# Performance work log

Measured on AMD Instinct MI355X. Metric: run time of the kernel, lower is better.

The kernel has to match this reference:

```python
import jax, jax.numpy as jnp
import numpy as np

POOL_SIZE = 100
TOP_K = 5
EPS = 1e-12

def l2_normalize(x, axis):
    # matches module: x * rsqrt(max(sum(x^2), eps))
    sq = jnp.sum(x * x, axis=axis, keepdims=True)
    return x * jax.lax.rsqrt(jnp.maximum(sq, EPS))

def setup_inputs() -> dict:
    key = jax.random.key(0)
    k1, k2 = jax.random.split(key)
    x_embed = jax.random.normal(k1, (256, 512, 768), dtype=jnp.float32)
    # prompt_key init 'uniform' -> U(-1, 1)
    prompt_key = jax.random.uniform(k2, (POOL_SIZE, 768), dtype=jnp.float32, minval=-1.0, maxval=1.0)
    return {"x_embed": x_embed, "prompt_key": prompt_key}

def reference(x_embed, prompt_key):
    B = x_embed.shape[0]
    # embedding_key == 'cls' with cls_features=None -> max over sequence dim
    x_embed_mean = jnp.max(x_embed, axis=1)                      # [B, D]
    prompt_norm = l2_normalize(prompt_key, axis=1)               # [P, D]
    x_embed_norm = l2_normalize(x_embed_mean, axis=1)            # [B, D]
    similarity = jnp.matmul(x_embed_norm, prompt_norm.T)         # [B, P]
    _, idx = jax.lax.top_k(similarity, TOP_K)                    # [B, K] (batchwise_prompt=False)
    selected_key = prompt_norm[idx]                              # [B, K, D] gather
    sim = selected_key * x_embed_norm[:, None, :]                # [B, K, D]
    reduce_sim = jnp.sum(sim) / B
    return similarity, selected_key, reduce_sim, idx
```

## Files before the change

kernel.cpp:

```cpp
#include <hip/hip_runtime.h>
#include <float.h>

#define B 256
#define S 512
#define D 768
#define P 100
#define K 5
#define SPLIT 4
#define SCHUNK (S / SPLIT)
#define D4 (D / 4)

#define PART_OFF 0
#define PN_OFF   (SPLIT * B * D)
#define XN_OFF   (PN_OFF + P * D)

#define SIM_OFF 0
#define SEL_OFF (B * P)
#define RS_OFF  (SEL_OFF + B * K * D)
#define IDX_OFF (RS_OFF + 1)

__device__ inline float4 fmax4(float4 a, float4 b) {
    return make_float4(fmaxf(a.x, b.x), fmaxf(a.y, b.y),
                       fmaxf(a.z, b.z), fmaxf(a.w, b.w));
}

__global__ __launch_bounds__(192) void k_partmax(const float* __restrict__ x,
                                                 float* __restrict__ ws) {
    const int blk = blockIdx.x;
    const int b  = blk >> 2;
    const int sp = blk & 3;
    const int t  = threadIdx.x;
    const float4* src = (const float4*)(x + (size_t)b * S * D)
                        + (size_t)(sp * SCHUNK) * D4 + t;
    float4 m0 = make_float4(-FLT_MAX, -FLT_MAX, -FLT_MAX, -FLT_MAX);
    float4 m1 = m0, m2 = m0, m3 = m0;
    for (int s = 0; s < SCHUNK; s += 4) {
        float4 a0 = src[(size_t)(s + 0) * D4];
        float4 a1 = src[(size_t)(s + 1) * D4];
        float4 a2 = src[(size_t)(s + 2) * D4];
        float4 a3 = src[(size_t)(s + 3) * D4];
        m0 = fmax4(m0, a0);
        m1 = fmax4(m1, a1);
        m2 = fmax4(m2, a2);
        m3 = fmax4(m3, a3);
    }
    float4 m = fmax4(fmax4(m0, m1), fmax4(m2, m3));
    ((float4*)(ws + PART_OFF))[(size_t)(sp * B + b) * D4 + t] = m;
}

__device__ inline float block_sum_192(float v, float* lds) {
    for (int off = 32; off; off >>= 1) v += __shfl_down(v, off);
    const int lane = threadIdx.x & 63;
    const int w = threadIdx.x >> 6;
    if (lane == 0) lds[w] = v;
    __syncthreads();
    float tot = lds[0] + lds[1] + lds[2];
    __syncthreads();
    return tot;
}

__device__ inline float precise_rsqrt(float tot) {
    float x = fmaxf(tot, 1e-12f);
    float r = rsqrtf(x);
    r = r * (1.5f - 0.5f * x * r * r);
    return r;
}

__global__ __launch_bounds__(192) void k_prompt_norm(const float* __restrict__ pk,
                                                     float* __restrict__ ws) {
    __shared__ float lds[3];
    const int p = blockIdx.x, t = threadIdx.x;
    float4 v = ((const float4*)pk)[(size_t)p * D4 + t];
    float sq = v.x * v.x + v.y * v.y + v.z * v.z + v.w * v.w;
    float tot = block_sum_192(sq, lds);
    float r = precise_rsqrt(tot);
    ((float4*)(ws + PN_OFF))[(size_t)p * D4 + t] =
        make_float4(v.x * r, v.y * r, v.z * r, v.w * r);
}

__global__ __launch_bounds__(192) void k_xnorm(float* __restrict__ ws,
                                               float* __restrict__ out) {
    __shared__ float lds[3];
    const int b = blockIdx.x, t = threadIdx.x;
    const float4* part = (const float4*)(ws + PART_OFF);
    float4 m = part[(size_t)b * D4 + t];
    for (int sp = 1; sp < SPLIT; ++sp)
        m = fmax4(m, part[(size_t)(sp * B + b) * D4 + t]);
    float sq = m.x * m.x + m.y * m.y + m.z * m.z + m.w * m.w;
    float tot = block_sum_192(sq, lds);
    float r = precise_rsqrt(tot);
    ((float4*)(ws + XN_OFF))[(size_t)b * D4 + t] =
        make_float4(m.x * r, m.y * r, m.z * r, m.w * r);
    if (b == 0 && t == 0) out[RS_OFF] = 0.0f;
}

__global__ __launch_bounds__(256) void k_sim_topk(const float* __restrict__ ws,
                                                  float* __restrict__ out) {
    __shared__ float xs[D];
    __shared__ float simbuf[P];
    __shared__ float topv[K];
    __shared__ int   topi[K];
    const int b = blockIdx.x, t = threadIdx.x;
    const int w = t >> 6, lane = t & 63;

    const float* xn = ws + XN_OFF + (size_t)b * D;
    if (t < D4) ((float4*)xs)[t] = ((const float4*)xn)[t];
    __syncthreads();

    const float* pn = ws + PN_OFF;
    for (int j = 0; j < 25; ++j) {
        const int p = w + 4 * j;
        float acc = 0.f;
        #pragma unroll
        for (int jj = 0; jj < 12; ++jj) {
            const int d = lane + 64 * jj;
            acc += pn[(size_t)p * D + d] * xs[d];
        }
        for (int off = 32; off; off >>= 1) acc += __shfl_down(acc, off);
        if (lane == 0) {
            simbuf[p] = acc;
            out[SIM_OFF + (size_t)b * P + p] = acc;
        }
    }
    __syncthreads();

    if (w == 0) {
        float v0 = (lane < P) ? simbuf[lane] : -FLT_MAX;
        int   i0 = lane;
        int   i1 = lane + 64;
        float v1 = (i1 < P) ? simbuf[i1] : -FLT_MAX;
        for (int k = 0; k < K; ++k) {
            float bv; int bi;
            if (v0 > v1 || (v0 == v1 && i0 < i1)) { bv = v0; bi = i0; }
            else                                  { bv = v1; bi = i1; }
            for (int off = 32; off; off >>= 1) {
                float ov = __shfl_xor(bv, off);
                int   oi = __shfl_xor(bi, off);
                if (ov > bv || (ov == bv && oi < bi)) { bv = ov; bi = oi; }
            }
            if (lane == 0) { topv[k] = bv; topi[k] = bi; }
            if (bi == i0) v0 = -FLT_MAX;
            else if (bi == i1) v1 = -FLT_MAX;
        }
    }
    __syncthreads();

    if (t < K) out[IDX_OFF + (size_t)b * K + t] = (float)topi[t];

    if (t == 0) {
        float s = topv[0] + topv[1] + topv[2] + topv[3] + topv[4];
        atomicAdd(out + RS_OFF, s * (1.0f / (float)B));
    }

    const float4* pn4 = (const float4*)pn;
    float4* sel4 = (float4*)(out + SEL_OFF) + (size_t)b * (K * D4);
    for (int i = t; i < K * D4; i += 256) {
        const int k = i / D4;
        const int e = i - k * D4;
        sel4[i] = pn4[(size_t)topi[k] * D4 + e];
    }
}

extern "C" void kernel_launch(void* const* d_in, const int* in_sizes, int n_in,
                              void* d_out, int out_size, void* d_ws, size_t ws_size,
                              hipStream_t stream) {
    const float* x_embed    = (const float*)d_in[0];
    const float* prompt_key = (const float*)d_in[1];
    float* out = (float*)d_out;
    float* ws  = (float*)d_ws;

    k_partmax<<<B * SPLIT, 192, 0, stream>>>(x_embed, ws);
    k_prompt_norm<<<P, 192, 0, stream>>>(prompt_key, ws);
    k_xnorm<<<B, 192, 0, stream>>>(ws, out);
    k_sim_topk<<<B, 256, 0, stream>>>(ws, out);
}
```

Baseline: 611.4 us.

## Fuse x-normalization into similarity/top-k kernel and double sequence split

The x-normalization kernel is merged into the similarity/top-k kernel, so each block reduces the partial maxima and normalizes its row directly in shared memory. This removes one launch and one round trip through the workspace. The sequence split for the max reduction goes from 4 to 8, giving 2048 blocks for the bandwidth-bound pass, and the fused kernel now reads 8 partial vectors per row. The prompt-norm kernel now runs first and zeroes the reduce_sim accumulator.

```diff
diff --git a/kernel.cpp b/kernel.cpp
--- a/kernel.cpp
+++ b/kernel.cpp
@@ -6,13 +6,12 @@
 #define D 768
 #define P 100
 #define K 5
-#define SPLIT 4
+#define SPLIT 8
 #define SCHUNK (S / SPLIT)
 #define D4 (D / 4)
 
 #define PART_OFF 0
 #define PN_OFF   (SPLIT * B * D)
-#define XN_OFF   (PN_OFF + P * D)
 
 #define SIM_OFF 0
 #define SEL_OFF (B * P)
@@ -24,11 +23,36 @@
                        fmaxf(a.z, b.z), fmaxf(a.w, b.w));
 }
 
+__device__ inline float precise_rsqrt(float tot) {
+    float x = fmaxf(tot, 1e-12f);
+    float r = rsqrtf(x);
+    r = r * (1.5f - 0.5f * x * r * r);
+    return r;
+}
+
+__global__ __launch_bounds__(192) void k_prompt_norm(const float* __restrict__ pk,
+                                                     float* __restrict__ ws,
+                                                     float* __restrict__ out) {
+    __shared__ float lds[3];
+    const int p = blockIdx.x, t = threadIdx.x;
+    float4 v = ((const float4*)pk)[(size_t)p * D4 + t];
+    float sq = v.x * v.x + v.y * v.y + v.z * v.z + v.w * v.w;
+    for (int off = 32; off; off >>= 1) sq += __shfl_down(sq, off);
+    const int lane = t & 63, w = t >> 6;
+    if (lane == 0) lds[w] = sq;
+    __syncthreads();
+    float tot = lds[0] + lds[1] + lds[2];
+    float r = precise_rsqrt(tot);
+    ((float4*)(ws + PN_OFF))[(size_t)p * D4 + t] =
+        make_float4(v.x * r, v.y * r, v.z * r, v.w * r);
+    if (p == 0 && t == 0) out[RS_OFF] = 0.0f;
+}
+
 __global__ __launch_bounds__(192) void k_partmax(const float* __restrict__ x,
                                                  float* __restrict__ ws) {
     const int blk = blockIdx.x;
-    const int b  = blk >> 2;
-    const int sp = blk & 3;
+    const int b  = blk >> 3;
+    const int sp = blk & 7;
     const int t  = threadIdx.x;
     const float4* src = (const float4*)(x + (size_t)b * S * D)
                         + (size_t)(sp * SCHUNK) * D4 + t;
@@ -48,63 +72,33 @@
     ((float4*)(ws + PART_OFF))[(size_t)(sp * B + b) * D4 + t] = m;
 }
 
-__device__ inline float block_sum_192(float v, float* lds) {
-    for (int off = 32; off; off >>= 1) v += __shfl_down(v, off);
-    const int lane = threadIdx.x & 63;
-    const int w = threadIdx.x >> 6;
-    if (lane == 0) lds[w] = v;
-    __syncthreads();
-    float tot = lds[0] + lds[1] + lds[2];
-    __syncthreads();
-    return tot;
-}
-
-__device__ inline float precise_rsqrt(float tot) {
-    float x = fmaxf(tot, 1e-12f);
-    float r = rsqrtf(x);
-    r = r * (1.5f - 0.5f * x * r * r);
-    return r;
-}
-
-__global__ __launch_bounds__(192) void k_prompt_norm(const float* __restrict__ pk,
-                                                     float* __restrict__ ws) {
-    __shared__ float lds[3];
-    const int p = blockIdx.x, t = threadIdx.x;
-    float4 v = ((const float4*)pk)[(size_t)p * D4 + t];
-    float sq = v.x * v.x + v.y * v.y + v.z * v.z + v.w * v.w;
-    float tot = block_sum_192(sq, lds);
-    float r = precise_rsqrt(tot);
-    ((float4*)(ws + PN_OFF))[(size_t)p * D4 + t] =
-        make_float4(v.x * r, v.y * r, v.z * r, v.w * r);
-}
-
-__global__ __launch_bounds__(192) void k_xnorm(float* __restrict__ ws,
+__global__ __launch_bounds__(256) void k_fused(const float* __restrict__ ws,
                                                float* __restrict__ out) {
-    __shared__ float lds[3];
-    const int b = blockIdx.x, t = threadIdx.x;
-    const float4* part = (const float4*)(ws + PART_OFF);
-    float4 m = part[(size_t)b * D4 + t];
-    for (int sp = 1; sp < SPLIT; ++sp)
-        m = fmax4(m, part[(size_t)(sp * B + b) * D4 + t]);
-    float sq = m.x * m.x + m.y * m.y + m.z * m.z + m.w * m.w;
-    float tot = block_sum_192(sq, lds);
-    float r = precise_rsqrt(tot);
-    ((float4*)(ws + XN_OFF))[(size_t)b * D4 + t] =
-        make_float4(m.x * r, m.y * r, m.z * r, m.w * r);
-    if (b == 0 && t == 0) out[RS_OFF] = 0.0f;
-}
-
-__global__ __launch_bounds__(256) void k_sim_topk(const float* __restrict__ ws,
-                                                  float* __restrict__ out) {
     __shared__ float xs[D];
     __shared__ float simbuf[P];
+    __shared__ float lds[4];
     __shared__ float topv[K];
     __shared__ int   topi[K];
     const int b = blockIdx.x, t = threadIdx.x;
     const int w = t >> 6, lane = t & 63;
 
-    const float* xn = ws + XN_OFF + (size_t)b * D;
-    if (t < D4) ((float4*)xs)[t] = ((const float4*)xn)[t];
+    float4 m = make_float4(0.f, 0.f, 0.f, 0.f);
+    float sq = 0.f;
+    if (t < D4) {
+        const float4* part = (const float4*)(ws + PART_OFF);
+        m = part[(size_t)b * D4 + t];
+        #pragma unroll
+        for (int sp = 1; sp < SPLIT; ++sp)
+            m = fmax4(m, part[(size_t)(sp * B + b) * D4 + t]);
+        sq = m.x * m.x + m.y * m.y + m.z * m.z + m.w * m.w;
+    }
+    for (int off = 32; off; off >>= 1) sq += __shfl_down(sq, off);
+    if (lane == 0) lds[w] = sq;
+    __syncthreads();
+    float tot = lds[0] + lds[1] + lds[2] + lds[3];
+    float r = precise_rsqrt(tot);
+    if (t < D4)
+        ((float4*)xs)[t] = make_float4(m.x * r, m.y * r, m.z * r, m.w * r);
     __syncthreads();
 
     const float* pn = ws + PN_OFF;
@@ -169,8 +163,7 @@
     float* out = (float*)d_out;
     float* ws  = (float*)d_ws;
 
+    k_prompt_norm<<<P, 192, 0, stream>>>(prompt_key, ws, out);
     k_partmax<<<B * SPLIT, 192, 0, stream>>>(x_embed, ws);
-    k_prompt_norm<<<P, 192, 0, stream>>>(prompt_key, ws);
-    k_xnorm<<<B, 192, 0, stream>>>(ws, out);
-    k_sim_topk<<<B, 256, 0, stream>>>(ws, out);
+    k_fused<<<B, 256, 0, stream>>>(ws, out);
 }
```

Result: slower. 637.9 us (+4.3%).
